# Kernel tuning notes

Hardware: AMD Instinct MI355X
Metric: run time of the kernel (lower is better)

Reference implementation:

```python
import jax, jax.numpy as jnp
import numpy as np

NEG_SLOPE = 0.2  # leaky_relu_negative_slope


def setup_inputs() -> dict:
    key = jax.random.key(0)
    k = jax.random.split(key, 6)
    N = 1024          # n_nodes == nei_nodes (forced by the asserts in forward)
    IN = 256          # in_features
    OUT = 256         # out_features (nei_embedding feature dim, since linear_r = Linear(out_features, ...))
    H, F = 4, 64      # n_heads, n_hidden = out_features // n_heads
    h = jax.random.normal(k[0], (N, IN), dtype=jnp.float32)
    nei_embedding = jax.random.normal(k[1], (N, OUT), dtype=jnp.float32)
    adj_mat = jax.random.randint(k[2], (N, N), 0, 2).astype(jnp.float32)
    scale = 0.05
    w_l = jax.random.normal(k[3], (IN, H * F), dtype=jnp.float32) * scale   # linear_l.weight.T
    w_r = jax.random.normal(k[4], (OUT, H * F), dtype=jnp.float32) * scale  # linear_r.weight.T
    attn_w = jax.random.normal(k[5], (F,), dtype=jnp.float32) * scale       # attn.weight (1, F) -> (F,)
    return {"h": h, "nei_embedding": nei_embedding, "adj_mat": adj_mat,
            "w_l": w_l, "w_r": w_r, "attn_w": attn_w, "use_elu": 1}


def reference(h, nei_embedding, adj_mat, w_l, w_r, attn_w, use_elu):
    N = h.shape[0]
    M = nei_embedding.shape[0]
    F = attn_w.shape[0]
    H = w_l.shape[1] // F
    g_l = (h @ w_l).reshape(N, H, F)              # (N, H, F)
    g_r = (nei_embedding @ w_r).reshape(M, H, F)  # (M, H, F)
    # Torch does repeat/repeat_interleave then view(n, m, H, F); with the
    # assert-enforced n == m this is exactly g_sum[i, j] = g_l[j] + g_r[i].
    g_sum = g_r[:, None, :, :] + g_l[None, :, :, :]          # (N, N, H, F)
    e = jnp.einsum("nmhf,f->nmh", jax.nn.leaky_relu(g_sum, NEG_SLOPE), attn_w)
    adj_t = adj_mat.T[:, :, None]                             # (M, N, 1) -> broadcasts over heads
    e = jnp.where(adj_t == 0, -jnp.inf, e)
    exp_attention = jnp.exp(e)
    weighted = exp_attention * adj_t                          # (N, N, H)
    denom = jnp.sum(weighted, axis=1, keepdims=True)
    a = weighted / denom                                      # masked softmax over neighbors
    # dropout is identity at inference
    attn_res = jnp.einsum("ijh,jhf->ihf", a, g_r)            # (N, H, F)
    if use_elu:
        attn_res = jax.nn.elu(attn_res)
    return attn_res.reshape(N, H * F)  # is_concat=True
```

## Files before the change

### kernel.cpp

```cpp
#include <hip/hip_runtime.h>
#include <math.h>

#define NN 1024
#define KK 256
#define NH 4
#define FD 64
#define HF 256

__global__ __launch_bounds__(256) void gatv2_gemm(
    const float* __restrict__ h, const float* __restrict__ nei,
    const float* __restrict__ w_l, const float* __restrict__ w_r,
    float* __restrict__ g_l, float* __restrict__ g_r)
{
    const float* A; const float* W; float* G;
    if (blockIdx.z == 0) { A = h;   W = w_l; G = g_l; }
    else                 { A = nei; W = w_r; G = g_r; }

    __shared__ float sA[32][36];
    __shared__ float sW[32][64];

    const int t  = threadIdx.x;
    const int tn = t & 15;
    const int tm = t >> 4;
    const int n0 = blockIdx.x * 64;
    const int m0 = blockIdx.y * 32;

    float acc0[4] = {0,0,0,0}, acc1[4] = {0,0,0,0};

    for (int kc = 0; kc < KK; kc += 32) {
        const int ar = t >> 3, ac = (t & 7) << 2;
        float4 va = *(const float4*)&A[(size_t)(m0 + ar)*KK + kc + ac];
        const int wc = (t & 15) << 2, wr = t >> 4;
        float4 v0 = *(const float4*)&W[(size_t)(kc + wr)*HF + n0 + wc];
        float4 v1 = *(const float4*)&W[(size_t)(kc + wr + 16)*HF + n0 + wc];
        __syncthreads();
        *(float4*)&sA[ar][ac]    = va;
        *(float4*)&sW[wr][wc]    = v0;
        *(float4*)&sW[wr+16][wc] = v1;
        __syncthreads();
        #pragma unroll
        for (int k = 0; k < 32; ++k) {
            float a0 = sA[tm*2][k];
            float a1 = sA[tm*2+1][k];
            float4 w4 = *(const float4*)&sW[k][tn<<2];
            acc0[0] += a0*w4.x; acc0[1] += a0*w4.y; acc0[2] += a0*w4.z; acc0[3] += a0*w4.w;
            acc1[0] += a1*w4.x; acc1[1] += a1*w4.y; acc1[2] += a1*w4.z; acc1[3] += a1*w4.w;
        }
    }
    const int m = m0 + tm*2, n = n0 + (tn<<2);
    *(float4*)&G[(size_t)m*HF + n]     = make_float4(acc0[0],acc0[1],acc0[2],acc0[3]);
    *(float4*)&G[(size_t)(m+1)*HF + n] = make_float4(acc1[0],acc1[1],acc1[2],acc1[3]);
}

__global__ __launch_bounds__(256, 2) void gatv2_attn(
    const float* __restrict__ g_l, const float* __restrict__ g_r,
    const float* __restrict__ adj, const float* __restrict__ attn_w,
    float* __restrict__ accP, float* __restrict__ denP,
    int JPB, int SC)
{
    extern __shared__ float sh[];
    float* s_gl = sh;
    float* s_gr = sh + SC*FD;
    float* s_cl = sh + 2*SC*FD;

    const int t     = threadIdx.x;
    const int jcIdx = blockIdx.x;
    const int ib    = blockIdx.y;
    const int hh    = blockIdx.z;
    const int i     = ib*256 + t;

    float4 wa[16];
    {
        const float4* wp = (const float4*)attn_w;
        #pragma unroll
        for (int q = 0; q < 16; ++q) {
            float4 w = wp[q];
            wa[q] = make_float4(w.x*0.4f, w.y*0.4f, w.z*0.4f, w.w*0.4f);
        }
    }
    float4 gri[16];
    float cr = 0.f;
    {
        const float4* gp = (const float4*)(g_r + (size_t)i*HF + hh*FD);
        #pragma unroll
        for (int q = 0; q < 16; ++q) {
            gri[q] = gp[q];
            cr += wa[q].x*gri[q].x + wa[q].y*gri[q].y + wa[q].z*gri[q].z + wa[q].w*gri[q].w;
        }
        cr *= 1.5f;
    }
    float4 acc[16];
    #pragma unroll
    for (int q = 0; q < 16; ++q) acc[q] = make_float4(0.f,0.f,0.f,0.f);
    float denom = 0.f;

    const int jbase = jcIdx * JPB;
    for (int s0 = 0; s0 < JPB; s0 += SC) {
        const int j0 = jbase + s0;
        __syncthreads();
        for (int p = t; p < SC*16; p += 256) {
            const int jr = p >> 4, c = (p & 15) << 2;
            *(float4*)&s_gl[jr*FD + c] = *(const float4*)&g_l[(size_t)(j0 + jr)*HF + hh*FD + c];
            *(float4*)&s_gr[jr*FD + c] = *(const float4*)&g_r[(size_t)(j0 + jr)*HF + hh*FD + c];
        }
        __syncthreads();
        if (t < SC) {
            float s = 0.f;
            const float* row = &s_gl[t*FD];
            #pragma unroll
            for (int q = 0; q < 16; ++q)
                s += wa[q].x*row[4*q] + wa[q].y*row[4*q+1] + wa[q].z*row[4*q+2] + wa[q].w*row[4*q+3];
            s_cl[t] = 1.5f*s;
        }
        __syncthreads();

        float mask_next = adj[(size_t)j0*NN + i];
        for (int jj = 0; jj < SC; ++jj) {
            const float mask = mask_next;
            if (jj + 1 < SC) mask_next = adj[(size_t)(j0 + jj + 1)*NN + i];
            const float clj = s_cl[jj];
            const float4* glr = (const float4*)&s_gl[jj*FD];
            float e0 = 0.f, e1 = 0.f, e2 = 0.f, e3 = 0.f;
            #pragma unroll
            for (int q = 0; q < 16; ++q) {
                float4 g = glr[q];
                e0 += wa[q].x * fabsf(g.x + gri[q].x);
                e1 += wa[q].y * fabsf(g.y + gri[q].y);
                e2 += wa[q].z * fabsf(g.z + gri[q].z);
                e3 += wa[q].w * fabsf(g.w + gri[q].w);
            }
            const float e = cr + clj + ((e0+e1)+(e2+e3));
            const float pw = (mask != 0.f) ? __expf(e) : 0.f;
            denom += pw;
            const float4* grr = (const float4*)&s_gr[jj*FD];
            #pragma unroll
            for (int q = 0; q < 16; ++q) {
                float4 g = grr[q];
                acc[q].x += pw*g.x; acc[q].y += pw*g.y;
                acc[q].z += pw*g.z; acc[q].w += pw*g.w;
            }
        }
    }
    float* op = accP + (size_t)jcIdx*(NN*HF) + ((size_t)i*NH + hh)*FD;
    #pragma unroll
    for (int q = 0; q < 16; ++q) ((float4*)op)[q] = acc[q];
    denP[(size_t)jcIdx*(NN*NH) + (size_t)i*NH + hh] = denom;
}

__global__ __launch_bounds__(256) void gatv2_reduce(
    const float* __restrict__ accP, const float* __restrict__ denP,
    const int* __restrict__ use_elu, float* __restrict__ out, int NC)
{
    const int idx = blockIdx.x*256 + threadIdx.x;
    float s = 0.f, d = 0.f;
    for (int c = 0; c < NC; ++c) {
        s += accP[(size_t)c*(NN*HF) + idx];
        d += denP[(size_t)c*(NN*NH) + (idx >> 6)];
    }
    float r = s / d;
    if (*use_elu != 0) r = (r > 0.f) ? r : expm1f(r);
    out[idx] = r;
}

extern "C" void kernel_launch(void* const* d_in, const int* in_sizes, int n_in,
                              void* d_out, int out_size, void* d_ws, size_t ws_size,
                              hipStream_t stream)
{
    const float* h    = (const float*)d_in[0];
    const float* nei  = (const float*)d_in[1];
    const float* adj  = (const float*)d_in[2];
    const float* w_l  = (const float*)d_in[3];
    const float* w_r  = (const float*)d_in[4];
    const float* aw   = (const float*)d_in[5];
    const int*   uel  = (const int*)d_in[6];
    float* out = (float*)d_out;
    float* ws  = (float*)d_ws;

    float* g_l = ws;
    float* g_r = ws + (size_t)NN*HF;

    int NC = 32;
    while (NC > 1) {
        size_t need = ((size_t)2*NN*HF + (size_t)NC*NN*NH + (size_t)NC*NN*HF) * sizeof(float);
        if (need <= ws_size) break;
        NC >>= 1;
    }
    const int JPB = NN / NC;
    const int SC  = JPB < 64 ? JPB : 64;

    float* denP = g_r + (size_t)NN*HF;
    float* accP = denP + (size_t)NC*NN*NH;

    hipLaunchKernelGGL(gatv2_gemm, dim3(HF/64, NN/32, 2), dim3(256), 0, stream,
                       h, nei, w_l, w_r, g_l, g_r);
    const size_t shb = (size_t)(2*SC*FD + SC) * sizeof(float);
    hipLaunchKernelGGL(gatv2_attn, dim3(NC, NN/256, NH), dim3(256), shb, stream,
                       g_l, g_r, adj, aw, accP, denP, JPB, SC);
    hipLaunchKernelGGL(gatv2_reduce, dim3((NN*HF)/256), dim3(256), 0, stream,
                       accP, denP, uel, out, NC);
}
```

Before: 151.6 us.

## Drop LDS staging in attention kernel, precompute left scores, enlarge GEMM tile

The attention kernel no longer stages g_l/g_r rows in shared memory with barriers. It reads them straight from global memory; they are uniform across the block and likely served by scalar or L1 cache. The per-row left attention score is now computed once by a new small kernel rather than per block. The projection GEMM moves to a 64x64 tile with 4x4 per-thread outputs and a transposed A tile for better reuse. The risks are redundant global and cache traffic in the hot j-loop and one extra kernel launch.

Result: slower. 171.0 us (+12.8%).

```diff
diff --git a/kernel.cpp b/kernel.cpp
--- a/kernel.cpp
+++ b/kernel.cpp
@@ -16,135 +16,130 @@
     if (blockIdx.z == 0) { A = h;   W = w_l; G = g_l; }
     else                 { A = nei; W = w_r; G = g_r; }
 
-    __shared__ float sA[32][36];
-    __shared__ float sW[32][64];
+    __shared__ float sA[16][68];
+    __shared__ float sW[16][64];
 
-    const int t  = threadIdx.x;
-    const int tn = t & 15;
-    const int tm = t >> 4;
-    const int n0 = blockIdx.x * 64;
-    const int m0 = blockIdx.y * 32;
+    const int t   = threadIdx.x;
+    const int tm4 = (t >> 4) << 2;
+    const int tn4 = (t & 15) << 2;
+    const int m0  = blockIdx.y * 64;
+    const int n0  = blockIdx.x * 64;
 
-    float acc0[4] = {0,0,0,0}, acc1[4] = {0,0,0,0};
+    float acc[4][4] = {};
 
-    for (int kc = 0; kc < KK; kc += 32) {
-        const int ar = t >> 3, ac = (t & 7) << 2;
-        float4 va = *(const float4*)&A[(size_t)(m0 + ar)*KK + kc + ac];
-        const int wc = (t & 15) << 2, wr = t >> 4;
-        float4 v0 = *(const float4*)&W[(size_t)(kc + wr)*HF + n0 + wc];
-        float4 v1 = *(const float4*)&W[(size_t)(kc + wr + 16)*HF + n0 + wc];
+    const int ar = t >> 2, ac = (t & 3) << 2;
+    const int wr = t >> 4, wc = (t & 15) << 2;
+
+    for (int k0 = 0; k0 < KK; k0 += 16) {
+        float4 va = *(const float4*)&A[(size_t)(m0 + ar)*KK + k0 + ac];
+        float4 vw = *(const float4*)&W[(size_t)(k0 + wr)*HF + n0 + wc];
         __syncthreads();
-        *(float4*)&sA[ar][ac]    = va;
-        *(float4*)&sW[wr][wc]    = v0;
-        *(float4*)&sW[wr+16][wc] = v1;
+        sA[ac+0][ar] = va.x; sA[ac+1][ar] = va.y;
+        sA[ac+2][ar] = va.z; sA[ac+3][ar] = va.w;
+        *(float4*)&sW[wr][wc] = vw;
         __syncthreads();
         #pragma unroll
-        for (int k = 0; k < 32; ++k) {
-            float a0 = sA[tm*2][k];
-            float a1 = sA[tm*2+1][k];
-            float4 w4 = *(const float4*)&sW[k][tn<<2];
-            acc0[0] += a0*w4.x; acc0[1] += a0*w4.y; acc0[2] += a0*w4.z; acc0[3] += a0*w4.w;
-            acc1[0] += a1*w4.x; acc1[1] += a1*w4.y; acc1[2] += a1*w4.z; acc1[3] += a1*w4.w;
+        for (int kk = 0; kk < 16; ++kk) {
+            float4 a4 = *(const float4*)&sA[kk][tm4];
+            float4 w4 = *(const float4*)&sW[kk][tn4];
+            const float am[4] = {a4.x, a4.y, a4.z, a4.w};
+            const float wn[4] = {w4.x, w4.y, w4.z, w4.w};
+            #pragma unroll
+            for (int mi = 0; mi < 4; ++mi)
+                #pragma unroll
+                for (int ni = 0; ni < 4; ++ni)
+                    acc[mi][ni] += am[mi] * wn[ni];
         }
     }
-    const int m = m0 + tm*2, n = n0 + (tn<<2);
-    *(float4*)&G[(size_t)m*HF + n]     = make_float4(acc0[0],acc0[1],acc0[2],acc0[3]);
-    *(float4*)&G[(size_t)(m+1)*HF + n] = make_float4(acc1[0],acc1[1],acc1[2],acc1[3]);
+    #pragma unroll
+    for (int mi = 0; mi < 4; ++mi)
+        *(float4*)&G[(size_t)(m0 + tm4 + mi)*HF + n0 + tn4] =
+            make_float4(acc[mi][0], acc[mi][1], acc[mi][2], acc[mi][3]);
+}
+
+__global__ __launch_bounds__(256) void gatv2_cl(
+    const float* __restrict__ g_l, const float* __restrict__ aw, float* __restrict__ cl)
+{
+    const int idx = blockIdx.x*256 + threadIdx.x;
+    const int j = idx >> 2, hh = idx & 3;
+    const float4* row = (const float4*)(g_l + (size_t)j*HF + hh*FD);
+    const float4* wp  = (const float4*)aw;
+    float s = 0.f;
+    #pragma unroll
+    for (int q = 0; q < 16; ++q) {
+        float4 g = row[q], w = wp[q];
+        s += g.x*w.x + g.y*w.y + g.z*w.z + g.w*w.w;
+    }
+    cl[idx] = 0.6f * s;
 }
 
 __global__ __launch_bounds__(256, 2) void gatv2_attn(
     const float* __restrict__ g_l, const float* __restrict__ g_r,
     const float* __restrict__ adj, const float* __restrict__ attn_w,
-    float* __restrict__ accP, float* __restrict__ denP,
-    int JPB, int SC)
+    const float* __restrict__ cl,
+    float* __restrict__ accP, float* __restrict__ denP, int JPB)
 {
-    extern __shared__ float sh[];
-    float* s_gl = sh;
-    float* s_gr = sh + SC*FD;
-    float* s_cl = sh + 2*SC*FD;
+    const int t  = threadIdx.x;
+    const int jc = blockIdx.x;
+    const int ib = blockIdx.y;
+    const int hh = blockIdx.z;
+    const int i  = ib*256 + t;
 
-    const int t     = threadIdx.x;
-    const int jcIdx = blockIdx.x;
-    const int ib    = blockIdx.y;
-    const int hh    = blockIdx.z;
-    const int i     = ib*256 + t;
+    const float4* wp = (const float4*)attn_w;
 
-    float4 wa[16];
-    {
-        const float4* wp = (const float4*)attn_w;
-        #pragma unroll
-        for (int q = 0; q < 16; ++q) {
-            float4 w = wp[q];
-            wa[q] = make_float4(w.x*0.4f, w.y*0.4f, w.z*0.4f, w.w*0.4f);
-        }
-    }
     float4 gri[16];
-    float cr = 0.f;
+    float crdot = 0.f;
     {
         const float4* gp = (const float4*)(g_r + (size_t)i*HF + hh*FD);
         #pragma unroll
         for (int q = 0; q < 16; ++q) {
-            gri[q] = gp[q];
-            cr += wa[q].x*gri[q].x + wa[q].y*gri[q].y + wa[q].z*gri[q].z + wa[q].w*gri[q].w;
+            float4 g = gp[q], w = wp[q];
+            gri[q] = g;
+            crdot += w.x*g.x + w.y*g.y + w.z*g.z + w.w*g.w;
         }
-        cr *= 1.5f;
     }
+    const float cr = 0.6f * crdot;
+
     float4 acc[16];
     #pragma unroll
     for (int q = 0; q < 16; ++q) acc[q] = make_float4(0.f,0.f,0.f,0.f);
     float denom = 0.f;
 
-    const int jbase = jcIdx * JPB;
-    for (int s0 = 0; s0 < JPB; s0 += SC) {
-        const int j0 = jbase + s0;
-        __syncthreads();
-        for (int p = t; p < SC*16; p += 256) {
-            const int jr = p >> 4, c = (p & 15) << 2;
-            *(float4*)&s_gl[jr*FD + c] = *(const float4*)&g_l[(size_t)(j0 + jr)*HF + hh*FD + c];
-            *(float4*)&s_gr[jr*FD + c] = *(const float4*)&g_r[(size_t)(j0 + jr)*HF + hh*FD + c];
+    const int jbase = jc * JPB;
+    const float* glh = g_l + (size_t)hh*FD;
+    const float* grh = g_r + (size_t)hh*FD;
+
+    float mask_next = adj[(size_t)jbase*NN + i];
+    for (int jj = 0; jj < JPB; ++jj) {
+        const int j = jbase + jj;
+        const float mask = mask_next;
+        if (jj + 1 < JPB) mask_next = adj[(size_t)(j + 1)*NN + i];
+        const float clj = cl[j*NH + hh];
+        const float4* glr = (const float4*)(glh + (size_t)j*HF);
+        float e0 = 0.f, e1 = 0.f, e2 = 0.f, e3 = 0.f;
+        #pragma unroll
+        for (int q = 0; q < 16; ++q) {
+            float4 g = glr[q], w = wp[q];
+            e0 += w.x * fabsf(g.x + gri[q].x);
+            e1 += w.y * fabsf(g.y + gri[q].y);
+            e2 += w.z * fabsf(g.z + gri[q].z);
+            e3 += w.w * fabsf(g.w + gri[q].w);
         }
-        __syncthreads();
-        if (t < SC) {
-            float s = 0.f;
-            const float* row = &s_gl[t*FD];
-            #pragma unroll
-            for (int q = 0; q < 16; ++q)
-                s += wa[q].x*row[4*q] + wa[q].y*row[4*q+1] + wa[q].z*row[4*q+2] + wa[q].w*row[4*q+3];
-            s_cl[t] = 1.5f*s;
-        }
-        __syncthreads();
-
-        float mask_next = adj[(size_t)j0*NN + i];
-        for (int jj = 0; jj < SC; ++jj) {
-            const float mask = mask_next;
-            if (jj + 1 < SC) mask_next = adj[(size_t)(j0 + jj + 1)*NN + i];
-            const float clj = s_cl[jj];
-            const float4* glr = (const float4*)&s_gl[jj*FD];
-            float e0 = 0.f, e1 = 0.f, e2 = 0.f, e3 = 0.f;
-            #pragma unroll
-            for (int q = 0; q < 16; ++q) {
-                float4 g = glr[q];
-                e0 += wa[q].x * fabsf(g.x + gri[q].x);
-                e1 += wa[q].y * fabsf(g.y + gri[q].y);
-                e2 += wa[q].z * fabsf(g.z + gri[q].z);
-                e3 += wa[q].w * fabsf(g.w + gri[q].w);
-            }
-            const float e = cr + clj + ((e0+e1)+(e2+e3));
-            const float pw = (mask != 0.f) ? __expf(e) : 0.f;
-            denom += pw;
-            const float4* grr = (const float4*)&s_gr[jj*FD];
-            #pragma unroll
-            for (int q = 0; q < 16; ++q) {
-                float4 g = grr[q];
-                acc[q].x += pw*g.x; acc[q].y += pw*g.y;
-                acc[q].z += pw*g.z; acc[q].w += pw*g.w;
-            }
+        const float e = cr + clj + 0.4f * ((e0+e1) + (e2+e3));
+        const float pw = (mask != 0.f) ? __expf(e) : 0.f;
+        denom += pw;
+        const float4* grr = (const float4*)(grh + (size_t)j*HF);
+        #pragma unroll
+        for (int q = 0; q < 16; ++q) {
+            float4 g = grr[q];
+            acc[q].x += pw*g.x; acc[q].y += pw*g.y;
+            acc[q].z += pw*g.z; acc[q].w += pw*g.w;
         }
     }
-    float* op = accP + (size_t)jcIdx*(NN*HF) + ((size_t)i*NH + hh)*FD;
+    float* op = accP + (size_t)jc*(NN*HF) + ((size_t)i*NH + hh)*FD;
     #pragma unroll
     for (int q = 0; q < 16; ++q) ((float4*)op)[q] = acc[q];
-    denP[(size_t)jcIdx*(NN*NH) + (size_t)i*NH + hh] = denom;
+    denP[(size_t)jc*(NN*NH) + (size_t)i*NH + hh] = denom;
 }
 
 __global__ __launch_bounds__(256) void gatv2_reduce(
@@ -177,25 +172,27 @@
     float* ws  = (float*)d_ws;
 
     float* g_l = ws;
-    float* g_r = ws + (size_t)NN*HF;
+    float* g_r = g_l + (size_t)NN*HF;
+    float* cl  = g_r + (size_t)NN*HF;
 
     int NC = 32;
     while (NC > 1) {
-        size_t need = ((size_t)2*NN*HF + (size_t)NC*NN*NH + (size_t)NC*NN*HF) * sizeof(float);
+        size_t need = ((size_t)2*NN*HF + (size_t)NN*NH
+                     + (size_t)NC*NN*NH + (size_t)NC*NN*HF) * sizeof(float);
         if (need <= ws_size) break;
         NC >>= 1;
     }
     const int JPB = NN / NC;
-    const int SC  = JPB < 64 ? JPB : 64;
 
-    float* denP = g_r + (size_t)NN*HF;
+    float* denP = cl + (size_t)NN*NH;
     float* accP = denP + (size_t)NC*NN*NH;
 
-    hipLaunchKernelGGL(gatv2_gemm, dim3(HF/64, NN/32, 2), dim3(256), 0, stream,
+    hipLaunchKernelGGL(gatv2_gemm, dim3(HF/64, NN/64, 2), dim3(256), 0, stream,
                        h, nei, w_l, w_r, g_l, g_r);
-    const size_t shb = (size_t)(2*SC*FD + SC) * sizeof(float);
-    hipLaunchKernelGGL(gatv2_attn, dim3(NC, NN/256, NH), dim3(256), shb, stream,
-                       g_l, g_r, adj, aw, accP, denP, JPB, SC);
+    hipLaunchKernelGGL(gatv2_cl, dim3((NN*NH)/256), dim3(256), 0, stream,
+                       g_l, aw, cl);
+    hipLaunchKernelGGL(gatv2_attn, dim3(NC, NN/256, NH), dim3(256), 0, stream,
+                       g_l, g_r, adj, aw, cl, accP, denP, JPB);
     hipLaunchKernelGGL(gatv2_reduce, dim3((NN*HF)/256), dim3(256), 0, stream,
                        accP, denP, uel, out, NC);
 }
```
